# Kernel optimization log

Measured on AMD Instinct MI355X. Metric: run time of the kernel, lower is better.

## Reference

```python
import jax, jax.numpy as jnp
from jax import lax
import numpy as np

B, C, T, D = 262144, 3, 10, 5
H = 8  # per-direction hidden size


def setup_inputs() -> dict:
    key = jax.random.key(0)
    ks = jax.random.split(key, 7)
    s = 1.0 / np.sqrt(H)  # pytorch default uniform(-1/sqrt(H),1/sqrt(H)); use scaled normal
    return {
        "x": jax.random.normal(ks[0], (B, C, T, D), jnp.float32),
        "Wih0": jax.random.normal(ks[1], (2, 4 * H, C * D), jnp.float32) * s,
        "Wih_rest": jax.random.normal(ks[2], (2, 2, 4 * H, 2 * H), jnp.float32) * s,
        "Whh": jax.random.normal(ks[3], (3, 2, 4 * H, H), jnp.float32) * s,
        "b": jax.random.normal(ks[4], (3, 2, 4 * H), jnp.float32) * s,  # b_ih + b_hh combined
        "Wout": jax.random.normal(ks[5], (1, 2 * H * T), jnp.float32) * 0.05,
        "bout": jnp.zeros((1,), jnp.float32),
    }


def _lstm_dir(h_in, Wih, Whh_d, b_d, reverse):
    # h_in: [B,T,Din]; precompute input projections for all timesteps at once
    xg = jnp.einsum('btd,gd->btg', h_in, Wih) + b_d  # [B,T,4H]

    def step(carry, xt):
        h, c = carry
        g = xt + h @ Whh_d.T  # [B,4H]
        i, f, gg, o = jnp.split(g, 4, axis=-1)  # pytorch gate order i,f,g,o
        i = jax.nn.sigmoid(i)
        f = jax.nn.sigmoid(f)
        gg = jnp.tanh(gg)
        o = jax.nn.sigmoid(o)
        c = f * c + i * gg
        h = o * jnp.tanh(c)
        return (h, c), h

    nb = h_in.shape[0]
    h0 = jnp.zeros((nb, H), h_in.dtype)
    _, ys = lax.scan(step, (h0, h0), jnp.swapaxes(xg, 0, 1), reverse=reverse)
    return jnp.swapaxes(ys, 0, 1)  # [B,T,H]


def reference(x, Wih0, Wih_rest, Whh, b, Wout, bout):
    # x: [B,C,T,D] -> [B,T,C*D]
    h = jnp.transpose(x, (0, 2, 1, 3)).reshape(x.shape[0], T, C * D)
    for l in range(3):
        Wf = Wih0[0] if l == 0 else Wih_rest[l - 1, 0]
        Wb = Wih0[1] if l == 0 else Wih_rest[l - 1, 1]
        fwd = _lstm_dir(h, Wf, Whh[l, 0], b[l, 0], False)
        bwd = _lstm_dir(h, Wb, Whh[l, 1], b[l, 1], True)
        h = jnp.concatenate([fwd, bwd], axis=-1)  # [B,T,2H]
    flat = h.reshape(h.shape[0], T * 2 * H)  # [B,160]
    out = flat @ Wout.T + bout  # [B,1]
    return out.squeeze()
```

## Files before the change

### kernel.cpp

```cpp
#include <hip/hip_runtime.h>

#define TPB 256

typedef float f32x2 __attribute__((ext_vector_type(2)));
typedef float f32x4 __attribute__((ext_vector_type(4)));
typedef short s16x8 __attribute__((ext_vector_type(8)));

#define L2E 1.44269504f
#define PKFMA(acc, w, xx) asm("v_pk_fma_f32 %0, %1, %2, %0" : "+v"(acc) : "v"(w), "v"(xx))
#define PKMUL(dst, w, xx) asm("v_pk_mul_f32 %0, %1, %2" : "=v"(dst) : "v"(w), "v"(xx))

__device__ __forceinline__ unsigned pack_split(float v) {
    unsigned b  = __float_as_uint(v);
    unsigned hi = b >> 16;
    float    hf = __uint_as_float(b & 0xFFFF0000u);
    unsigned lob = __float_as_uint(v - hf) & 0xFFFF0000u;
    return lob | hi;
}

__device__ __forceinline__ void build_seg(int l, int dir,
        const float* __restrict__ Wih0, const float* __restrict__ Wih_rest,
        const float* __restrict__ Whh,  const float* __restrict__ bW,
        unsigned* __restrict__ sBF, float* __restrict__ sWh,
        float* __restrict__ sBias, int tid)
{
    const int seg = l * 2 + dir;
    {
        const int lane_ = tid & 63, part = (tid >> 6) & 1, nt = tid >> 7;
        const int u  = nt * 16 + (lane_ & 15);
        const float sc = ((u >> 3) == 2) ? (-2.0f * L2E) : (-L2E);
        #pragma unroll
        for (int ip = 0; ip < 4; ++ip) {
            const int d = (lane_ >> 4) * 4 + ip;
            float w;
            if (l == 0) w = (d < 15) ? Wih0[dir * 480 + u * 15 + d] : 0.0f;
            else        w = Wih_rest[((l - 1) * 2 + dir) * 512 + u * 16 + d];
            w *= sc;
            unsigned b = __float_as_uint(w);
            unsigned v16;
            if (part == 0) v16 = b >> 16;
            else {
                float hf = __uint_as_float(b & 0xFFFF0000u);
                v16 = __float_as_uint(w - hf) >> 16;
            }
            sBF[((nt * 2 + part) * 64 + lane_) * 4 + ip] = v16 | (v16 << 16);
        }
    }
    {
        const int jj = tid >> 5, rr = tid & 31;
        const float sc = ((rr >> 3) == 2) ? (-2.0f * L2E) : (-L2E);
        const int u = (rr >> 3) * 8 + jj;
        sWh[jj * 36 + rr] = sc * Whh[seg * 256 + u * 8 + (rr & 7)];
    }
    if (tid < 32) {
        const float sc = ((tid >> 3) == 2) ? (-2.0f * L2E) : (-L2E);
        sBias[tid] = sc * bW[seg * 32 + tid];
    }
}

template<int DIR, bool LAST>
__device__ __forceinline__ void run_seg(const unsigned* __restrict__ XSin,
                                        unsigned* __restrict__ XSout,
                                        const unsigned* __restrict__ sBF,
                                        const float* __restrict__ sWh,
                                        const float* __restrict__ sBias,
                                        const float* __restrict__ sWout,
                                        float* __restrict__ G2,
                                        float* __restrict__ sH,
                                        float& accOut, int lane, int wid)
{
    const int r   = lane & 15;
    const int kb  = lane >> 4;
    const int grp = lane >> 3;
    const int j   = lane & 7;
    const int elg = wid * 8 + grp;

    s16x8 Bf00 = *(const s16x8*)&sBF[(0 * 64 + lane) * 4];
    s16x8 Bf01 = *(const s16x8*)&sBF[(1 * 64 + lane) * 4];
    s16x8 Bf10 = *(const s16x8*)&sBF[(2 * 64 + lane) * 4];
    s16x8 Bf11 = *(const s16x8*)&sBF[(3 * 64 + lane) * 4];
    const float bs0 = sBias[r];
    const float bs1 = sBias[16 + r];

    const int AI0 = ((r >> 3) * 32 + wid * 8 + (r & 7)) * 16 + kb * 4;
    const int tloc  = kb >> 1;
    const int base7 = (kb & 1) * 4;
    const int SBW = wid * 576 + tloc * 288 + base7 * 36 + r;
    const int GBW = wid * 576 + grp * 36 + j;

    float gx[4][10];
    #pragma unroll
    for (int m = 0; m < 5; ++m) {
        s16x8 A = *(const s16x8*)&XSin[AI0 + m * 1024];
        f32x4 acc0 = {bs0, bs0, bs0, bs0};
        f32x4 acc1 = {bs1, bs1, bs1, bs1};
        acc0 = __builtin_amdgcn_mfma_f32_16x16x32_bf16(A, Bf00, acc0, 0, 0, 0);
        acc0 = __builtin_amdgcn_mfma_f32_16x16x32_bf16(A, Bf01, acc0, 0, 0, 0);
        acc1 = __builtin_amdgcn_mfma_f32_16x16x32_bf16(A, Bf10, acc1, 0, 0, 0);
        acc1 = __builtin_amdgcn_mfma_f32_16x16x32_bf16(A, Bf11, acc1, 0, 0, 0);
        #pragma unroll
        for (int q = 0; q < 4; ++q) {
            G2[SBW + q * 36]      = acc0[q];
            G2[SBW + q * 36 + 16] = acc1[q];
        }
        #pragma unroll
        for (int t2 = 0; t2 < 2; ++t2)
            #pragma unroll
            for (int g = 0; g < 4; ++g)
                gx[g][2 * m + t2] = G2[GBW + t2 * 288 + g * 8];
    }

    f32x2 whp[16];
    #pragma unroll
    for (int g = 0; g < 4; ++g)
        #pragma unroll
        for (int kp = 0; kp < 4; ++kp)
            whp[g * 4 + kp] = *(const f32x2*)&sWh[j * 36 + g * 8 + kp * 2];

    float cst = 0.0f, hn = 0.0f;
    const int hbase = wid * 64 + grp * 8;
    #pragma unroll
    for (int tt = 0; tt < 10; ++tt) {
        const int s = DIR ? (9 - tt) : tt;
        float g0 = gx[0][s], g1 = gx[1][s], g2v = gx[2][s], g3 = gx[3][s];
        if (tt > 0) {
            f32x2 h01 = *(const f32x2*)&sH[hbase];
            f32x2 h23 = *(const f32x2*)&sH[hbase + 2];
            f32x2 h45 = *(const f32x2*)&sH[hbase + 4];
            f32x2 h67 = *(const f32x2*)&sH[hbase + 6];
            f32x2 a0, a1, a2, a3;
            PKMUL(a0, whp[0],  h01); PKFMA(a0, whp[1],  h23); PKFMA(a0, whp[2],  h45); PKFMA(a0, whp[3],  h67);
            PKMUL(a1, whp[4],  h01); PKFMA(a1, whp[5],  h23); PKFMA(a1, whp[6],  h45); PKFMA(a1, whp[7],  h67);
            PKMUL(a2, whp[8],  h01); PKFMA(a2, whp[9],  h23); PKFMA(a2, whp[10], h45); PKFMA(a2, whp[11], h67);
            PKMUL(a3, whp[12], h01); PKFMA(a3, whp[13], h23); PKFMA(a3, whp[14], h45); PKFMA(a3, whp[15], h67);
            g0 += a0.x + a0.y; g1 += a1.x + a1.y;
            g2v += a2.x + a2.y; g3 += a3.x + a3.y;
        }
        const float ig = __builtin_amdgcn_rcpf(1.0f + __builtin_amdgcn_exp2f(g0));
        const float fg = __builtin_amdgcn_rcpf(1.0f + __builtin_amdgcn_exp2f(g1));
        const float gg = 2.0f * __builtin_amdgcn_rcpf(1.0f + __builtin_amdgcn_exp2f(g2v)) - 1.0f;
        const float og = __builtin_amdgcn_rcpf(1.0f + __builtin_amdgcn_exp2f(g3));
        cst = fg * cst + ig * gg;
        const float ec = __builtin_amdgcn_exp2f(-2.0f * L2E * cst);
        const float th = 2.0f * __builtin_amdgcn_rcpf(1.0f + ec) - 1.0f;
        hn = og * th;

        if (tt < 9) sH[hbase + j] = hn;
        if (LAST) accOut += hn * sWout[s * 16 + DIR * 8 + j];
        else      XSout[((s * 32 + elg) << 4) + DIR * 8 + j] = pack_split(hn);
    }
}

__global__ __launch_bounds__(TPB, 2)
void lstm_kernel(const float* __restrict__ x,
                 const float* __restrict__ Wih0,
                 const float* __restrict__ Wih_rest,
                 const float* __restrict__ Whh,
                 const float* __restrict__ bW,
                 const float* __restrict__ Wout,
                 const float* __restrict__ bout,
                 float* __restrict__ out)
{
    __shared__ __align__(16) unsigned XA[5120];
    __shared__ __align__(16) unsigned XB[5120];
    __shared__ __align__(16) float    G2[2304];
    __shared__ __align__(16) float    sH[256];
    __shared__ __align__(16) unsigned sBF[1024];
    __shared__ __align__(16) float    sWh[288];
    __shared__             float      sBias[32];
    __shared__             float      sWoutS[160];

    const int tid = threadIdx.x;
    if (tid < 160) sWoutS[tid] = Wout[tid];

    const float* xblk = x + (size_t)blockIdx.x * (32 * 150);
    for (int i = tid; i < 4800; i += TPB) {
        int e = i / 150, rr = i % 150;
        int c = rr / 50, r2 = rr % 50, t = r2 / 5, d = r2 % 5;
        XA[((t * 32 + e) << 4) + c * 5 + d] = pack_split(xblk[i]);
    }
    for (int i = tid; i < 320; i += TPB) {
        int t = i >> 5, e = i & 31;
        XA[((t * 32 + e) << 4) + 15] = 0u;
    }
    build_seg(0, 0, Wih0, Wih_rest, Whh, bW, sBF, sWh, sBias, tid);

    const int lane = tid & 63, wid = tid >> 6;
    float accOut = 0.0f;

    __syncthreads();
    run_seg<0, false>(XA, XB, sBF, sWh, sBias, sWoutS, G2, sH, accOut, lane, wid);
    __syncthreads();
    build_seg(0, 1, Wih0, Wih_rest, Whh, bW, sBF, sWh, sBias, tid);
    __syncthreads();
    run_seg<1, false>(XA, XB, sBF, sWh, sBias, sWoutS, G2, sH, accOut, lane, wid);
    __syncthreads();
    build_seg(1, 0, Wih0, Wih_rest, Whh, bW, sBF, sWh, sBias, tid);
    __syncthreads();
    run_seg<0, false>(XB, XA, sBF, sWh, sBias, sWoutS, G2, sH, accOut, lane, wid);
    __syncthreads();
    build_seg(1, 1, Wih0, Wih_rest, Whh, bW, sBF, sWh, sBias, tid);
    __syncthreads();
    run_seg<1, false>(XB, XA, sBF, sWh, sBias, sWoutS, G2, sH, accOut, lane, wid);
    __syncthreads();
    build_seg(2, 0, Wih0, Wih_rest, Whh, bW, sBF, sWh, sBias, tid);
    __syncthreads();
    run_seg<0, true>(XA, XB, sBF, sWh, sBias, sWoutS, G2, sH, accOut, lane, wid);
    __syncthreads();
    build_seg(2, 1, Wih0, Wih_rest, Whh, bW, sBF, sWh, sBias, tid);
    __syncthreads();
    run_seg<1, true>(XA, XB, sBF, sWh, sBias, sWoutS, G2, sH, accOut, lane, wid);

    accOut += __shfl_xor(accOut, 1);
    accOut += __shfl_xor(accOut, 2);
    accOut += __shfl_xor(accOut, 4);
    if ((lane & 7) == 0)
        out[(size_t)blockIdx.x * 32 + wid * 8 + (lane >> 3)] = accOut + bout[0];
}

extern "C" void kernel_launch(void* const* d_in, const int* in_sizes, int n_in,
                              void* d_out, int out_size, void* d_ws, size_t ws_size,
                              hipStream_t stream) {
    const float* x        = (const float*)d_in[0];
    const float* Wih0     = (const float*)d_in[1];
    const float* Wih_rest = (const float*)d_in[2];
    const float* Whh      = (const float*)d_in[3];
    const float* b        = (const float*)d_in[4];
    const float* Wout     = (const float*)d_in[5];
    const float* bout     = (const float*)d_in[6];
    float* out = (float*)d_out;

    const int nblocks = out_size / 32;
    lstm_kernel<<<nblocks, TPB, 0, stream>>>(x, Wih0, Wih_rest, Whh, b, Wout, bout, out);
}
```

Before: 357.2 us.

## Precompute weights in prep kernel, make waves independent, swizzle hidden state

Weight packing, scaling and the recurrent weight transposition move into a separate one-block prep kernel that writes to workspace. The main kernel then reads per-segment weights straight from global memory, so all block-wide barriers between segments are gone and each wave processes its own 8 elements independently. The hidden state is exchanged through ds_swizzle xor lane permutes instead of round trips through LDS, with the recurrent weights pre-permuted to match. Input buffers are padded to a stride of 17 to reduce bank conflicts, and the launch bound is raised to 3 blocks per CU. The cost is an extra kernel launch, repeated global or L2 weight loads per wave, and more scalar FMAs and swizzles per step.

```diff
diff --git a/kernel.cpp b/kernel.cpp
--- a/kernel.cpp
+++ b/kernel.cpp
@@ -1,14 +1,12 @@
 #include <hip/hip_runtime.h>
 
 #define TPB 256
-
-typedef float f32x2 __attribute__((ext_vector_type(2)));
+#define L2E 1.44269504f
+
 typedef float f32x4 __attribute__((ext_vector_type(4)));
 typedef short s16x8 __attribute__((ext_vector_type(8)));
 
-#define L2E 1.44269504f
-#define PKFMA(acc, w, xx) asm("v_pk_fma_f32 %0, %1, %2, %0" : "+v"(acc) : "v"(w), "v"(xx))
-#define PKMUL(dst, w, xx) asm("v_pk_mul_f32 %0, %1, %2" : "=v"(dst) : "v"(w), "v"(xx))
+#define SWZ(v, m) __int_as_float(__builtin_amdgcn_ds_swizzle(__float_as_int(v), ((m) << 10) | 31))
 
 __device__ __forceinline__ unsigned pack_split(float v) {
     unsigned b  = __float_as_uint(v);
@@ -18,55 +16,58 @@
     return lob | hi;
 }
 
-__device__ __forceinline__ void build_seg(int l, int dir,
-        const float* __restrict__ Wih0, const float* __restrict__ Wih_rest,
-        const float* __restrict__ Whh,  const float* __restrict__ bW,
-        unsigned* __restrict__ sBF, float* __restrict__ sWh,
-        float* __restrict__ sBias, int tid)
+__global__ void prep_kernel(const float* __restrict__ Wih0,
+                            const float* __restrict__ Wih_rest,
+                            const float* __restrict__ Whh,
+                            const float* __restrict__ bW,
+                            unsigned* __restrict__ wsBF,
+                            float* __restrict__ wsWH,
+                            float* __restrict__ wsBIAS)
 {
-    const int seg = l * 2 + dir;
-    {
-        const int lane_ = tid & 63, part = (tid >> 6) & 1, nt = tid >> 7;
-        const int u  = nt * 16 + (lane_ & 15);
-        const float sc = ((u >> 3) == 2) ? (-2.0f * L2E) : (-L2E);
-        #pragma unroll
-        for (int ip = 0; ip < 4; ++ip) {
-            const int d = (lane_ >> 4) * 4 + ip;
-            float w;
-            if (l == 0) w = (d < 15) ? Wih0[dir * 480 + u * 15 + d] : 0.0f;
-            else        w = Wih_rest[((l - 1) * 2 + dir) * 512 + u * 16 + d];
-            w *= sc;
-            unsigned b = __float_as_uint(w);
-            unsigned v16;
-            if (part == 0) v16 = b >> 16;
-            else {
-                float hf = __uint_as_float(b & 0xFFFF0000u);
-                v16 = __float_as_uint(w - hf) >> 16;
+    const int tid = threadIdx.x;
+    for (int seg = 0; seg < 6; ++seg) {
+        const int l = seg >> 1, dir = seg & 1;
+        {
+            const int lane_ = tid & 63, part = (tid >> 6) & 1, nt = tid >> 7;
+            const int u = nt * 16 + (lane_ & 15);
+            const float sc = ((u >> 3) == 2) ? (-2.0f * L2E) : (-L2E);
+            #pragma unroll
+            for (int ip = 0; ip < 4; ++ip) {
+                const int d = (lane_ >> 4) * 4 + ip;
+                float w;
+                if (l == 0) w = (d < 15) ? Wih0[dir * 480 + u * 15 + d] : 0.0f;
+                else        w = Wih_rest[((l - 1) * 2 + dir) * 512 + u * 16 + d];
+                w *= sc;
+                unsigned b = __float_as_uint(w);
+                unsigned v16;
+                if (part == 0) v16 = b >> 16;
+                else {
+                    float hf = __uint_as_float(b & 0xFFFF0000u);
+                    v16 = __float_as_uint(w - hf) >> 16;
+                }
+                wsBF[seg * 4096 + ((nt * 2 + part) * 64 + lane_) * 4 + ip] = v16 | (v16 << 16);
             }
-            sBF[((nt * 2 + part) * 64 + lane_) * 4 + ip] = v16 | (v16 << 16);
-        }
-    }
-    {
-        const int jj = tid >> 5, rr = tid & 31;
-        const float sc = ((rr >> 3) == 2) ? (-2.0f * L2E) : (-L2E);
-        const int u = (rr >> 3) * 8 + jj;
-        sWh[jj * 36 + rr] = sc * Whh[seg * 256 + u * 8 + (rr & 7)];
-    }
-    if (tid < 32) {
-        const float sc = ((tid >> 3) == 2) ? (-2.0f * L2E) : (-L2E);
-        sBias[tid] = sc * bW[seg * 32 + tid];
+        }
+        {
+            const int jj = tid >> 5, rr = tid & 31, g = rr >> 3, m = rr & 7;
+            const float sc = (g == 2) ? (-2.0f * L2E) : (-L2E);
+            wsWH[seg * 256 + jj * 32 + rr] = sc * Whh[seg * 256 + (g * 8 + jj) * 8 + (jj ^ m)];
+        }
+        if (tid < 32) {
+            const float sc = ((tid >> 3) == 2) ? (-2.0f * L2E) : (-L2E);
+            wsBIAS[seg * 32 + tid] = sc * bW[seg * 32 + tid];
+        }
     }
 }
 
 template<int DIR, bool LAST>
 __device__ __forceinline__ void run_seg(const unsigned* __restrict__ XSin,
                                         unsigned* __restrict__ XSout,
-                                        const unsigned* __restrict__ sBF,
-                                        const float* __restrict__ sWh,
-                                        const float* __restrict__ sBias,
-                                        const float* __restrict__ sWout,
+                                        const unsigned* __restrict__ bfSeg,
+                                        const float* __restrict__ whSeg,
+                                        const float* __restrict__ biasSeg,
+                                        const float* __restrict__ Wout,
                                         float* __restrict__ G2,
-                                        float* __restrict__ sH,
                                         float& accOut, int lane, int wid)
 {
     const int r   = lane & 15;
@@ -75,23 +76,21 @@
     const int j   = lane & 7;
     const int elg = wid * 8 + grp;
 
-    s16x8 Bf00 = *(const s16x8*)&sBF[(0 * 64 + lane) * 4];
-    s16x8 Bf01 = *(const s16x8*)&sBF[(1 * 64 + lane) * 4];
-    s16x8 Bf10 = *(const s16x8*)&sBF[(2 * 64 + lane) * 4];
-    s16x8 Bf11 = *(const s16x8*)&sBF[(3 * 64 + lane) * 4];
-    const float bs0 = sBias[r];
-    const float bs1 = sBias[16 + r];
-
-    const int AI0 = ((r >> 3) * 32 + wid * 8 + (r & 7)) * 16 + kb * 4;
-    const int tloc  = kb >> 1;
-    const int base7 = (kb & 1) * 4;
-    const int SBW = wid * 576 + tloc * 288 + base7 * 36 + r;
+    s16x8 Bf00 = *(const s16x8*)&bfSeg[(0 * 64 + lane) * 4];
+    s16x8 Bf01 = *(const s16x8*)&bfSeg[(1 * 64 + lane) * 4];
+    s16x8 Bf10 = *(const s16x8*)&bfSeg[(2 * 64 + lane) * 4];
+    s16x8 Bf11 = *(const s16x8*)&bfSeg[(3 * 64 + lane) * 4];
+    const float bs0 = biasSeg[r];
+    const float bs1 = biasSeg[16 + r];
+
+    const int AI0 = ((r >> 3) * 32 + wid * 8 + (r & 7)) * 17 + kb * 4;
+    const int SBW = wid * 576 + (kb >> 1) * 288 + (kb & 1) * 4 * 36 + r;
     const int GBW = wid * 576 + grp * 36 + j;
 
     float gx[4][10];
     #pragma unroll
     for (int m = 0; m < 5; ++m) {
-        s16x8 A = *(const s16x8*)&XSin[AI0 + m * 1024];
+        s16x8 A = *(const s16x8*)&XSin[AI0 + m * 1088];
         f32x4 acc0 = {bs0, bs0, bs0, bs0};
         f32x4 acc1 = {bs1, bs1, bs1, bs1};
         acc0 = __builtin_amdgcn_mfma_f32_16x16x32_bf16(A, Bf00, acc0, 0, 0, 0);
@@ -110,31 +109,35 @@
                 gx[g][2 * m + t2] = G2[GBW + t2 * 288 + g * 8];
     }
 
-    f32x2 whp[16];
+    float wh[32];
     #pragma unroll
-    for (int g = 0; g < 4; ++g)
-        #pragma unroll
-        for (int kp = 0; kp < 4; ++kp)
-            whp[g * 4 + kp] = *(const f32x2*)&sWh[j * 36 + g * 8 + kp * 2];
+    for (int q = 0; q < 8; ++q)
+        *(f32x4*)&wh[q * 4] = *(const f32x4*)&whSeg[j * 32 + q * 4];
 
     float cst = 0.0f, hn = 0.0f;
-    const int hbase = wid * 64 + grp * 8;
     #pragma unroll
     for (int tt = 0; tt < 10; ++tt) {
         const int s = DIR ? (9 - tt) : tt;
         float g0 = gx[0][s], g1 = gx[1][s], g2v = gx[2][s], g3 = gx[3][s];
         if (tt > 0) {
-            f32x2 h01 = *(const f32x2*)&sH[hbase];
-            f32x2 h23 = *(const f32x2*)&sH[hbase + 2];
-            f32x2 h45 = *(const f32x2*)&sH[hbase + 4];
-            f32x2 h67 = *(const f32x2*)&sH[hbase + 6];
-            f32x2 a0, a1, a2, a3;
-            PKMUL(a0, whp[0],  h01); PKFMA(a0, whp[1],  h23); PKFMA(a0, whp[2],  h45); PKFMA(a0, whp[3],  h67);
-            PKMUL(a1, whp[4],  h01); PKFMA(a1, whp[5],  h23); PKFMA(a1, whp[6],  h45); PKFMA(a1, whp[7],  h67);
-            PKMUL(a2, whp[8],  h01); PKFMA(a2, whp[9],  h23); PKFMA(a2, whp[10], h45); PKFMA(a2, whp[11], h67);
-            PKMUL(a3, whp[12], h01); PKFMA(a3, whp[13], h23); PKFMA(a3, whp[14], h45); PKFMA(a3, whp[15], h67);
-            g0 += a0.x + a0.y; g1 += a1.x + a1.y;
-            g2v += a2.x + a2.y; g3 += a3.x + a3.y;
+            const float h1 = SWZ(hn, 1), h2 = SWZ(hn, 2), h3 = SWZ(hn, 3),
+                        h4 = SWZ(hn, 4), h5 = SWZ(hn, 5), h6 = SWZ(hn, 6), h7 = SWZ(hn, 7);
+            g0 = fmaf(wh[0], hn, g0);  g0 = fmaf(wh[1], h1, g0);
+            g0 = fmaf(wh[2], h2, g0);  g0 = fmaf(wh[3], h3, g0);
+            g0 = fmaf(wh[4], h4, g0);  g0 = fmaf(wh[5], h5, g0);
+            g0 = fmaf(wh[6], h6, g0);  g0 = fmaf(wh[7], h7, g0);
+            g1 = fmaf(wh[8], hn, g1);  g1 = fmaf(wh[9], h1, g1);
+            g1 = fmaf(wh[10], h2, g1); g1 = fmaf(wh[11], h3, g1);
+            g1 = fmaf(wh[12], h4, g1); g1 = fmaf(wh[13], h5, g1);
+            g1 = fmaf(wh[14], h6, g1); g1 = fmaf(wh[15], h7, g1);
+            g2v = fmaf(wh[16], hn, g2v); g2v = fmaf(wh[17], h1, g2v);
+            g2v = fmaf(wh[18], h2, g2v); g2v = fmaf(wh[19], h3, g2v);
+            g2v = fmaf(wh[20], h4, g2v); g2v = fmaf(wh[21], h5, g2v);
+            g2v = fmaf(wh[22], h6, g2v); g2v = fmaf(wh[23], h7, g2v);
+            g3 = fmaf(wh[24], hn, g3);  g3 = fmaf(wh[25], h1, g3);
+            g3 = fmaf(wh[26], h2, g3);  g3 = fmaf(wh[27], h3, g3);
+            g3 = fmaf(wh[28], h4, g3);  g3 = fmaf(wh[29], h5, g3);
+            g3 = fmaf(wh[30], h6, g3);  g3 = fmaf(wh[31], h7, g3);
         }
         const float ig = __builtin_amdgcn_rcpf(1.0f + __builtin_amdgcn_exp2f(g0));
         const float fg = __builtin_amdgcn_rcpf(1.0f + __builtin_amdgcn_exp2f(g1));
@@ -145,71 +148,45 @@
         const float th = 2.0f * __builtin_amdgcn_rcpf(1.0f + ec) - 1.0f;
         hn = og * th;
 
-        if (tt < 9) sH[hbase + j] = hn;
-        if (LAST) accOut += hn * sWout[s * 16 + DIR * 8 + j];
-        else      XSout[((s * 32 + elg) << 4) + DIR * 8 + j] = pack_split(hn);
-    }
-}
-
-__global__ __launch_bounds__(TPB, 2)
+        if (LAST) accOut += hn * Wout[s * 16 + DIR * 8 + j];
+        else      XSout[(s * 32 + elg) * 17 + DIR * 8 + j] = pack_split(hn);
+    }
+}
+
+__global__ __launch_bounds__(TPB, 3)
 void lstm_kernel(const float* __restrict__ x,
-                 const float* __restrict__ Wih0,
-                 const float* __restrict__ Wih_rest,
-                 const float* __restrict__ Whh,
-                 const float* __restrict__ bW,
+                 const unsigned* __restrict__ wsBF,
+                 const float* __restrict__ wsWH,
+                 const float* __restrict__ wsBIAS,
                  const float* __restrict__ Wout,
                  const float* __restrict__ bout,
                  float* __restrict__ out)
 {
-    __shared__ __align__(16) unsigned XA[5120];
-    __shared__ __align__(16) unsigned XB[5120];
+    __shared__ __align__(16) unsigned XA[5440];
+    __shared__ __align__(16) unsigned XB[5440];
     __shared__ __align__(16) float    G2[2304];
-    __shared__ __align__(16) float    sH[256];
-    __shared__ __align__(16) unsigned sBF[1024];
-    __shared__ __align__(16) float    sWh[288];
-    __shared__             float      sBias[32];
-    __shared__             float      sWoutS[160];
-
-    const int tid = threadIdx.x;
-    if (tid < 160) sWoutS[tid] = Wout[tid];
-
-    const float* xblk = x + (size_t)blockIdx.x * (32 * 150);
-    for (int i = tid; i < 4800; i += TPB) {
-        int e = i / 150, rr = i % 150;
+
+    const int tid  = threadIdx.x;
+    const int lane = tid & 63, wid = tid >> 6;
+
+    const float* xw = x + (size_t)blockIdx.x * 4800 + wid * 1200;
+    for (int i = lane; i < 1200; i += 64) {
+        int e = wid * 8 + i / 150, rr = i % 150;
         int c = rr / 50, r2 = rr % 50, t = r2 / 5, d = r2 % 5;
-        XA[((t * 32 + e) << 4) + c * 5 + d] = pack_split(xblk[i]);
-    }
-    for (int i = tid; i < 320; i += TPB) {
-        int t = i >> 5, e = i & 31;
-        XA[((t * 32 + e) << 4) + 15] = 0u;
-    }
-    build_seg(0, 0, Wih0, Wih_rest, Whh, bW, sBF, sWh, sBias, tid);
-
-    const int lane = tid & 63, wid = tid >> 6;
+        XA[(t * 32 + e) * 17 + c * 5 + d] = pack_split(xw[i]);
+    }
+    for (int i = lane; i < 80; i += 64) {
+        int t = i >> 3, e = wid * 8 + (i & 7);
+        XA[(t * 32 + e) * 17 + 15] = 0u;
+    }
+
     float accOut = 0.0f;
-
-    __syncthreads();
-    run_seg<0, false>(XA, XB, sBF, sWh, sBias, sWoutS, G2, sH, accOut, lane, wid);
-    __syncthreads();
-    build_seg(0, 1, Wih0, Wih_rest, Whh, bW, sBF, sWh, sBias, tid);
-    __syncthreads();
-    run_seg<1, false>(XA, XB, sBF, sWh, sBias, sWoutS, G2, sH, accOut, lane, wid);
-    __syncthreads();
-    build_seg(1, 0, Wih0, Wih_rest, Whh, bW, sBF, sWh, sBias, tid);
-    __syncthreads();
-    run_seg<0, false>(XB, XA, sBF, sWh, sBias, sWoutS, G2, sH, accOut, lane, wid);
-    __syncthreads();
-    build_seg(1, 1, Wih0, Wih_rest, Whh, bW, sBF, sWh, sBias, tid);
-    __syncthreads();
-    run_seg<1, false>(XB, XA, sBF, sWh, sBias, sWoutS, G2, sH, accOut, lane, wid);
-    __syncthreads();
-    build_seg(2, 0, Wih0, Wih_rest, Whh, bW, sBF, sWh, sBias, tid);
-    __syncthreads();
-    run_seg<0, true>(XA, XB, sBF, sWh, sBias, sWoutS, G2, sH, accOut, lane, wid);
-    __syncthreads();
-    build_seg(2, 1, Wih0, Wih_rest, Whh, bW, sBF, sWh, sBias, tid);
-    __syncthreads();
-    run_seg<1, true>(XA, XB, sBF, sWh, sBias, sWoutS, G2, sH, accOut, lane, wid);
+    run_seg<0, false>(XA, XB, wsBF + 0 * 4096, wsWH + 0 * 256, wsBIAS + 0 * 32, Wout, G2, accOut, lane, wid);
+    run_seg<1, false>(XA, XB, wsBF + 1 * 4096, wsWH + 1 * 256, wsBIAS + 1 * 32, Wout, G2, accOut, lane, wid);
+    run_seg<0, false>(XB, XA, wsBF + 2 * 4096, wsWH + 2 * 256, wsBIAS + 2 * 32, Wout, G2, accOut, lane, wid);
+    run_seg<1, false>(XB, XA, wsBF + 3 * 4096, wsWH + 3 * 256, wsBIAS + 3 * 32, Wout, G2, accOut, lane, wid);
+    run_seg<0, true >(XA, XB, wsBF + 4 * 4096, wsWH + 4 * 256, wsBIAS + 4 * 32, Wout, G2, accOut, lane, wid);
+    run_seg<1, true >(XA, XB, wsBF + 5 * 4096, wsWH + 5 * 256, wsBIAS + 5 * 32, Wout, G2, accOut, lane, wid);
 
     accOut += __shfl_xor(accOut, 1);
     accOut += __shfl_xor(accOut, 2);
@@ -230,6 +207,12 @@
     const float* bout     = (const float*)d_in[6];
     float* out = (float*)d_out;
 
+    unsigned* wsBF   = (unsigned*)d_ws;
+    float*    wsWH   = (float*)d_ws + 6 * 4096;
+    float*    wsBIAS = (float*)d_ws + 6 * 4096 + 6 * 256;
+
+    prep_kernel<<<1, TPB, 0, stream>>>(Wih0, Wih_rest, Whh, b, wsBF, wsWH, wsBIAS);
+
     const int nblocks = out_size / 32;
-    lstm_kernel<<<nblocks, TPB, 0, stream>>>(x, Wih0, Wih_rest, Whh, b, Wout, bout, out);
-}
+    lstm_kernel<<<nblocks, TPB, 0, stream>>>(x, wsBF, wsWH, wsBIAS, Wout, bout, out);
+}
```

Result: faster. 295.1 us (-17.4%).
